# Kernel tuning notes

Hardware: AMD Instinct MI355X
Metric: run time of the kernel (lower is better)

## Reference

```python
import jax, jax.numpy as jnp
import numpy as np

IN_C = 256
INTER_C = 128


def _conv1x1(x_flat, w, b):
    # x_flat: [n, c_in, N]; w: [c_out, c_in]; b: [c_out] -> [n, c_out, N]
    return jnp.einsum('oc,bcn->bon', w, x_flat) + b[None, :, None]


def setup_inputs() -> dict:
    key = jax.random.key(0)
    ks = jax.random.split(key, 9)
    x = jax.random.normal(ks[0], (4, IN_C, 64, 64), dtype=jnp.float32)
    s_in = 1.0 / np.sqrt(IN_C)
    s_mid = 1.0 / np.sqrt(INTER_C)
    return {
        'x': x,
        'g_w': jax.random.uniform(ks[1], (INTER_C, IN_C), jnp.float32, -s_in, s_in),
        'g_b': jax.random.uniform(ks[2], (INTER_C,), jnp.float32, -s_in, s_in),
        'theta_w': jax.random.uniform(ks[3], (INTER_C, IN_C), jnp.float32, -s_in, s_in),
        'theta_b': jax.random.uniform(ks[4], (INTER_C,), jnp.float32, -s_in, s_in),
        'phi_w': jax.random.uniform(ks[5], (INTER_C, IN_C), jnp.float32, -s_in, s_in),
        'phi_b': jax.random.uniform(ks[6], (INTER_C,), jnp.float32, -s_in, s_in),
        'out_w': jax.random.uniform(ks[7], (IN_C, INTER_C), jnp.float32, -s_mid, s_mid),
        'out_b': jax.random.uniform(ks[8], (IN_C,), jnp.float32, -s_mid, s_mid),
    }


def reference(x, g_w, g_b, theta_w, theta_b, phi_w, phi_b, out_w, out_b):
    n, c, h, w = x.shape
    N = h * w
    x_flat = x.reshape(n, c, N)
    # 1x1-conv projections
    g_x = _conv1x1(x_flat, g_w, g_b).transpose(0, 2, 1)       # [n, N, ci]
    theta_x = _conv1x1(x_flat, theta_w, theta_b).transpose(0, 2, 1)  # [n, N, ci]
    phi_x = _conv1x1(x_flat, phi_w, phi_b)                    # [n, ci, N]
    # dot_product variant: pairwise weight normalized by N (no softmax)
    pairwise_weight = jnp.matmul(theta_x, phi_x) / N          # [n, N, N]
    y = jnp.matmul(pairwise_weight, g_x)                      # [n, N, ci]
    y = y.transpose(0, 2, 1)                                  # [n, ci, N]
    out = x_flat + _conv1x1(y, out_w, out_b)                  # residual
    return out.reshape(n, c, h, w)
```

## Files before the change

kernel.cpp:

```cpp
#include <hip/hip_runtime.h>
#include <hip/hip_bf16.h>


#define CC   256
#define NSP  4096
#define NB   4
#define KSPLIT 16

typedef __attribute__((ext_vector_type(8))) short bf16x8;
typedef __attribute__((ext_vector_type(4))) float f32x4;

#define F_WEND 1048576
#define H_PG   0
#define H_TT   4194304
#define H_S2   6291456

__device__ __forceinline__ unsigned short f2bf(float f) {
  __hip_bfloat16 h = __float2bfloat16(f);
  return __builtin_bit_cast(unsigned short, h);
}
__device__ __forceinline__ uint4 pack8(const unsigned short* h) {
  uint4 u;
  u.x = (unsigned)h[0] | ((unsigned)h[1] << 16);
  u.y = (unsigned)h[2] | ((unsigned)h[3] << 16);
  u.z = (unsigned)h[4] | ((unsigned)h[5] << 16);
  u.w = (unsigned)h[6] | ((unsigned)h[7] << 16);
  return u;
}
__device__ __forceinline__ bf16x8 ld_cvt8(const float* __restrict__ p) {
  float4 lo = *(const float4*)p;
  float4 hi = *(const float4*)(p + 4);
  bf16x8 r;
  r[0] = (short)f2bf(lo.x); r[1] = (short)f2bf(lo.y);
  r[2] = (short)f2bf(lo.z); r[3] = (short)f2bf(lo.w);
  r[4] = (short)f2bf(hi.x); r[5] = (short)f2bf(hi.y);
  r[6] = (short)f2bf(hi.z); r[7] = (short)f2bf(hi.w);
  return r;
}

__device__ __forceinline__ void wave_gemm_bt(const unsigned short* __restrict__ A, int pitchA,
                                             const unsigned short* __restrict__ B, int pitchB,
                                             int K, int lane, f32x4 acc[4][4]) {
  int lm = lane & 15, lq = lane >> 4;
  const unsigned short* ap[4];
  const unsigned short* bp[4];
#pragma unroll
  for (int i = 0; i < 4; ++i) {
    ap[i] = A + (size_t)(i * 16 + lm) * pitchA + lq * 8;
    bp[i] = B + (size_t)(i * 16 + lm) * pitchB + lq * 8;
  }
  bf16x8 a0[4], b0[4];
#pragma unroll
  for (int i = 0; i < 4; ++i) {
    a0[i] = *(const bf16x8*)(ap[i]);
    b0[i] = *(const bf16x8*)(bp[i]);
  }
  for (int k = 32; k < K; k += 32) {
    bf16x8 a1[4], b1[4];
#pragma unroll
    for (int i = 0; i < 4; ++i) {
      a1[i] = *(const bf16x8*)(ap[i] + k);
      b1[i] = *(const bf16x8*)(bp[i] + k);
    }
#pragma unroll
    for (int mi = 0; mi < 4; ++mi)
#pragma unroll
      for (int ni = 0; ni < 4; ++ni)
        acc[mi][ni] = __builtin_amdgcn_mfma_f32_16x16x32_bf16(a0[mi], b0[ni], acc[mi][ni], 0, 0, 0);
#pragma unroll
    for (int i = 0; i < 4; ++i) { a0[i] = a1[i]; b0[i] = b1[i]; }
  }
#pragma unroll
  for (int mi = 0; mi < 4; ++mi)
#pragma unroll
    for (int ni = 0; ni < 4; ++ni)
      acc[mi][ni] = __builtin_amdgcn_mfma_f32_16x16x32_bf16(a0[mi], b0[ni], acc[mi][ni], 0, 0, 0);
}

__global__ __launch_bounds__(256) void kP(
    const float* __restrict__ g_w, const float* __restrict__ theta_w,
    const float* __restrict__ phi_w, const float* __restrict__ g_b,
    const float* __restrict__ theta_b, const float* __restrict__ phi_b,
    const float* __restrict__ x, unsigned short* __restrict__ wsh) {
  __shared__ float T[64][65];
  __shared__ unsigned short XL[128 * 256];
  __shared__ float biasL[384];
  int bid = blockIdx.x;
  int b = bid >> 5, c = bid & 31;
  int t = threadIdx.x;
  if (t < 128) {
    biasL[t]       = g_b[t];
    biasL[128 + t] = theta_b[t];
    biasL[256 + t] = phi_b[t];
  }
  for (int s = 0; s < 8; ++s) {
    int kb = s >> 1, nb = s & 1;
    int r = t >> 2, j = t & 3;
    const float* xr = x + ((size_t)b * CC + kb * 64 + r) * NSP + c * 128 + nb * 64 + j * 16;
    float4 f0 = *(const float4*)(xr);
    float4 f1 = *(const float4*)(xr + 4);
    float4 f2 = *(const float4*)(xr + 8);
    float4 f3 = *(const float4*)(xr + 12);
    *(float4*)&T[r][j * 16 + 0]  = f0;
    *(float4*)&T[r][j * 16 + 4]  = f1;
    *(float4*)&T[r][j * 16 + 8]  = f2;
    *(float4*)&T[r][j * 16 + 12] = f3;
    __syncthreads();
    int nr = t >> 2, j2 = t & 3;
    unsigned short o[16];
#pragma unroll
    for (int i = 0; i < 16; ++i) o[i] = f2bf(T[j2 * 16 + i][nr]);
    int row = nb * 64 + nr;
    int kidx = kb * 64 + j2 * 16;
    int sw = (row & 7) << 3;
    *(uint4*)(XL + ((row * 256 + kidx) ^ sw))     = pack8(o);
    *(uint4*)(XL + ((row * 256 + kidx + 8) ^ sw)) = pack8(o + 8);
    __syncthreads();
  }

  int w = t >> 6, lane = t & 63;
  int wm = w >> 1, wn = w & 1;
  int lm = lane & 15, lq = lane >> 4;
  int bsw = (lm & 7) << 3;
#pragma unroll
  for (int r = 0; r < 3; ++r) {
    const float* wptr = (r == 0) ? g_w : (r == 1) ? theta_w : phi_w;
    const float* ap[4];
    int bidx[4];
#pragma unroll
    for (int i = 0; i < 4; ++i) {
      ap[i] = wptr + (size_t)(wm * 64 + i * 16 + lm) * CC + lq * 8;
      bidx[i] = (wn * 64 + i * 16 + lm) * 256 + lq * 8;
    }
    f32x4 acc[4][4] = {};
    bf16x8 a0[4], b0[4];
#pragma unroll
    for (int i = 0; i < 4; ++i) {
      a0[i] = ld_cvt8(ap[i]);
      b0[i] = *(const bf16x8*)(XL + (bidx[i] ^ bsw));
    }
    for (int k = 32; k < 256; k += 32) {
      bf16x8 a1[4], b1[4];
#pragma unroll
      for (int i = 0; i < 4; ++i) {
        a1[i] = ld_cvt8(ap[i] + k);
        b1[i] = *(const bf16x8*)(XL + ((bidx[i] + k) ^ bsw));
      }
#pragma unroll
      for (int mi = 0; mi < 4; ++mi)
#pragma unroll
        for (int ni = 0; ni < 4; ++ni)
          acc[mi][ni] = __builtin_amdgcn_mfma_f32_16x16x32_bf16(a0[mi], b0[ni], acc[mi][ni], 0, 0, 0);
#pragma unroll
      for (int i = 0; i < 4; ++i) { a0[i] = a1[i]; b0[i] = b1[i]; }
    }
#pragma unroll
    for (int mi = 0; mi < 4; ++mi)
#pragma unroll
      for (int ni = 0; ni < 4; ++ni)
        acc[mi][ni] = __builtin_amdgcn_mfma_f32_16x16x32_bf16(a0[mi], b0[ni], acc[mi][ni], 0, 0, 0);

    if (r == 1) {
      size_t tb = (size_t)b * 524288;
#pragma unroll
      for (int mi = 0; mi < 4; ++mi) {
        int p0 = wm * 64 + mi * 16 + lq * 4;
#pragma unroll
        for (int ni = 0; ni < 4; ++ni) {
          int n = c * 128 + wn * 64 + ni * 16 + lm;
          unsigned short u0 = f2bf(acc[mi][ni][0] + biasL[128 + p0 + 0]);
          unsigned short u1 = f2bf(acc[mi][ni][1] + biasL[128 + p0 + 1]);
          unsigned short u2 = f2bf(acc[mi][ni][2] + biasL[128 + p0 + 2]);
          unsigned short u3 = f2bf(acc[mi][ni][3] + biasL[128 + p0 + 3]);
          uint2 o;
          o.x = (unsigned)u0 | ((unsigned)u1 << 16);
          o.y = (unsigned)u2 | ((unsigned)u3 << 16);
          *(uint2*)(wsh + H_TT + tb + (size_t)n * 128 + p0) = o;
        }
      }
    } else {
      int rbase = (r == 0) ? 0 : 128;
      size_t pbo = (size_t)b * 1048576;
#pragma unroll
      for (int mi = 0; mi < 4; ++mi)
#pragma unroll
        for (int rr = 0; rr < 4; ++rr) {
          int rl = wm * 64 + mi * 16 + lq * 4 + rr;
          float bv = biasL[r * 128 + rl];
          size_t rowo = pbo + (size_t)(rbase + rl) * NSP;
#pragma unroll
          for (int ni = 0; ni < 4; ++ni)
            wsh[H_PG + rowo + c * 128 + wn * 64 + ni * 16 + lm] = f2bf(acc[mi][ni][rr] + bv);
        }
    }
  }
}

__global__ __launch_bounds__(256) void kS(const unsigned short* __restrict__ wsh,
                                          float* __restrict__ wsf) {
  int bid = blockIdx.x;
  int b = bid >> 4, ks = bid & 15;
  int t = threadIdx.x, w = t >> 6, lane = t & 63;
  int lm = lane & 15, lq = lane >> 4;
  int qm = w >> 1, qn = w & 1;
  const unsigned short* A = wsh + H_PG + (size_t)b * 1048576 +
                            (size_t)(128 + qm * 64) * NSP + ks * 256;
  const unsigned short* B = wsh + H_PG + (size_t)b * 1048576 +
                            (size_t)(qn * 64) * NSP + ks * 256;
  f32x4 acc[4][4] = {};
  wave_gemm_bt(A, NSP, B, NSP, 256, lane, acc);
  float* P = wsf + (size_t)(b * KSPLIT + ks) * 16384;
#pragma unroll
  for (int mi = 0; mi < 4; ++mi)
#pragma unroll
    for (int rr = 0; rr < 4; ++rr) {
      int p = qm * 64 + mi * 16 + lq * 4 + rr;
#pragma unroll
      for (int ni = 0; ni < 4; ++ni)
        P[p * 128 + qn * 64 + ni * 16 + lm] = acc[mi][ni][rr];
    }
}

__global__ __launch_bounds__(256) void kR(const float* __restrict__ wsf,
                                          unsigned short* __restrict__ wsh) {
  int bid = blockIdx.x;
  int b = bid >> 4, e = bid & 15;
  int t = threadIdx.x;
  int base = e * 1024 + t * 4;
  const float* PB = wsf + (size_t)b * KSPLIT * 16384;
  float4 s = {0.f, 0.f, 0.f, 0.f};
#pragma unroll
  for (int ks = 0; ks < KSPLIT; ++ks) {
    float4 p = *(const float4*)(PB + (size_t)ks * 16384 + base);
    s.x += p.x; s.y += p.y; s.z += p.z; s.w += p.w;
  }
  uint2 o;
  o.x = (unsigned)f2bf(s.x) | ((unsigned)f2bf(s.y) << 16);
  o.y = (unsigned)f2bf(s.z) | ((unsigned)f2bf(s.w) << 16);
  *(uint2*)(wsh + H_S2 + (size_t)b * 16384 + base) = o;
}

__global__ __launch_bounds__(256) void kD(const unsigned short* __restrict__ wsh,
                                          const float* __restrict__ out_w,
                                          const float* __restrict__ x,
                                          const float* __restrict__ out_b,
                                          float* __restrict__ out) {
  __shared__ unsigned short W2L[128 * 128];
  int bid = blockIdx.x;
  int b = bid >> 6, r6 = bid & 63;
  int tm = r6 >> 5, tn = r6 & 31;
  int t = threadIdx.x, w = t >> 6, lane = t & 63;
  int lm = lane & 15, lq = lane >> 4;
  int rb = tm * 128;

  {
    int pm = w >> 1, im = w & 1;
    const unsigned short* As = wsh + H_S2 + (size_t)b * 16384;
    f32x4 macc[4][4] = {};
    for (int kk = 0; kk < 128; kk += 32) {
      bf16x8 a[4], bb[4];
#pragma unroll
      for (int i = 0; i < 4; ++i) {
        a[i]  = *(const bf16x8*)(As + (size_t)(pm * 64 + i * 16 + lm) * 128 + lq * 8 + kk);
        bb[i] = ld_cvt8(out_w + (size_t)(rb + im * 64 + i * 16 + lm) * 128 + lq * 8 + kk);
      }
#pragma unroll
      for (int mi = 0; mi < 4; ++mi)
#pragma unroll
        for (int ni = 0; ni < 4; ++ni)
          macc[mi][ni] = __builtin_amdgcn_mfma_f32_16x16x32_bf16(a[mi], bb[ni], macc[mi][ni], 0, 0, 0);
    }
    const float inv = 1.0f / 4096.0f;
#pragma unroll
    for (int mi = 0; mi < 4; ++mi) {
      int p0 = pm * 64 + mi * 16 + lq * 4;
#pragma unroll
      for (int ni = 0; ni < 4; ++ni) {
        int il = im * 64 + ni * 16 + lm;
        unsigned short u0 = f2bf(macc[mi][ni][0] * inv);
        unsigned short u1 = f2bf(macc[mi][ni][1] * inv);
        unsigned short u2 = f2bf(macc[mi][ni][2] * inv);
        unsigned short u3 = f2bf(macc[mi][ni][3] * inv);
        uint2 o;
        o.x = (unsigned)u0 | ((unsigned)u1 << 16);
        o.y = (unsigned)u2 | ((unsigned)u3 << 16);
        *(uint2*)(W2L + ((il * 128 + p0) ^ ((il & 7) << 3))) = o;
      }
    }
  }
  __syncthreads();

  int wm = w >> 1, wn = w & 1;
  int cb = tn * 128 + wn * 64;
  int asw = (lm & 7) << 3;
  int aidx[4];
  const unsigned short* bp[4];
#pragma unroll
  for (int i = 0; i < 4; ++i) {
    aidx[i] = (wm * 64 + i * 16 + lm) * 128 + lq * 8;
    bp[i] = wsh + H_TT + (size_t)b * 524288 + (size_t)(cb + i * 16 + lm) * 128 + lq * 8;
  }
  f32x4 acc[4][4] = {};
  bf16x8 a0[4], b0[4];
#pragma unroll
  for (int i = 0; i < 4; ++i) {
    a0[i] = *(const bf16x8*)(W2L + (aidx[i] ^ asw));
    b0[i] = *(const bf16x8*)(bp[i]);
  }
  for (int k = 32; k < 128; k += 32) {
    bf16x8 a1[4], b1[4];
#pragma unroll
    for (int i = 0; i < 4; ++i) {
      a1[i] = *(const bf16x8*)(W2L + ((aidx[i] + k) ^ asw));
      b1[i] = *(const bf16x8*)(bp[i] + k);
    }
#pragma unroll
    for (int mi = 0; mi < 4; ++mi)
#pragma unroll
      for (int ni = 0; ni < 4; ++ni)
        acc[mi][ni] = __builtin_amdgcn_mfma_f32_16x16x32_bf16(a0[mi], b0[ni], acc[mi][ni], 0, 0, 0);
#pragma unroll
    for (int i = 0; i < 4; ++i) { a0[i] = a1[i]; b0[i] = b1[i]; }
  }
#pragma unroll
  for (int mi = 0; mi < 4; ++mi)
#pragma unroll
    for (int ni = 0; ni < 4; ++ni)
      acc[mi][ni] = __builtin_amdgcn_mfma_f32_16x16x32_bf16(a0[mi], b0[ni], acc[mi][ni], 0, 0, 0);

#pragma unroll
  for (int mi = 0; mi < 4; ++mi)
#pragma unroll
    for (int rr = 0; rr < 4; ++rr) {
      int row = rb + wm * 64 + mi * 16 + lq * 4 + rr;
      float bi = out_b[row];
#pragma unroll
      for (int ni = 0; ni < 4; ++ni) {
        int col = cb + ni * 16 + lm;
        size_t off = ((size_t)b * CC + row) * NSP + col;
        out[off] = acc[mi][ni][rr] + x[off] + bi;
      }
    }
}

extern "C" void kernel_launch(void* const* d_in, const int* in_sizes, int n_in,
                              void* d_out, int out_size, void* d_ws, size_t ws_size,
                              hipStream_t stream) {
  const float* x       = (const float*)d_in[0];
  const float* g_w     = (const float*)d_in[1];
  const float* g_b     = (const float*)d_in[2];
  const float* theta_w = (const float*)d_in[3];
  const float* theta_b = (const float*)d_in[4];
  const float* phi_w   = (const float*)d_in[5];
  const float* phi_b   = (const float*)d_in[6];
  const float* out_w   = (const float*)d_in[7];
  const float* out_b   = (const float*)d_in[8];
  float* wsf = (float*)d_ws;
  unsigned short* wsh = (unsigned short*)(wsf + F_WEND);
  float* out = (float*)d_out;

  kP<<<dim3(128), dim3(256), 0, stream>>>(g_w, theta_w, phi_w,
                                          g_b, theta_b, phi_b, x, wsh);
  kS<<<dim3(64), dim3(256), 0, stream>>>(wsh, wsf);
  kR<<<dim3(64), dim3(256), 0, stream>>>(wsf, wsh);
  kD<<<dim3(256), dim3(256), 0, stream>>>(wsh, out_w, x, out_b, out);
}
```

Baseline: 138.6 us.

## Fuse phi·g^T partial products into projection kernel, drop separate split-K kernel

The projection kernel now keeps its g and phi tiles in registers, stages them into shared memory, and computes the per-block 128x128 partial of phi·g^T directly, writing fp32 partials (32 splits, one per spatial chunk). This removes the bf16 g/phi round-trip through global memory and one kernel launch. The cost is more fp32 partial data for the reduction kernel to sum (KSPLIT doubles) and extra register and shared-memory pressure in kP.

```diff
diff --git a/kernel.cpp b/kernel.cpp
--- a/kernel.cpp
+++ b/kernel.cpp
@@ -5,15 +5,14 @@
 #define CC   256
 #define NSP  4096
 #define NB   4
-#define KSPLIT 16
+#define KSPLIT 32
 
 typedef __attribute__((ext_vector_type(8))) short bf16x8;
 typedef __attribute__((ext_vector_type(4))) float f32x4;
 
-#define F_WEND 1048576
-#define H_PG   0
-#define H_TT   4194304
-#define H_S2   6291456
+#define F_WEND 2097152
+#define H_TT   0
+#define H_S2   2097152
 
 __device__ __forceinline__ unsigned short f2bf(float f) {
   __hip_bfloat16 h = __float2bfloat16(f);
@@ -38,50 +37,12 @@
   return r;
 }
 
-__device__ __forceinline__ void wave_gemm_bt(const unsigned short* __restrict__ A, int pitchA,
-                                             const unsigned short* __restrict__ B, int pitchB,
-                                             int K, int lane, f32x4 acc[4][4]) {
-  int lm = lane & 15, lq = lane >> 4;
-  const unsigned short* ap[4];
-  const unsigned short* bp[4];
-#pragma unroll
-  for (int i = 0; i < 4; ++i) {
-    ap[i] = A + (size_t)(i * 16 + lm) * pitchA + lq * 8;
-    bp[i] = B + (size_t)(i * 16 + lm) * pitchB + lq * 8;
-  }
-  bf16x8 a0[4], b0[4];
-#pragma unroll
-  for (int i = 0; i < 4; ++i) {
-    a0[i] = *(const bf16x8*)(ap[i]);
-    b0[i] = *(const bf16x8*)(bp[i]);
-  }
-  for (int k = 32; k < K; k += 32) {
-    bf16x8 a1[4], b1[4];
-#pragma unroll
-    for (int i = 0; i < 4; ++i) {
-      a1[i] = *(const bf16x8*)(ap[i] + k);
-      b1[i] = *(const bf16x8*)(bp[i] + k);
-    }
-#pragma unroll
-    for (int mi = 0; mi < 4; ++mi)
-#pragma unroll
-      for (int ni = 0; ni < 4; ++ni)
-        acc[mi][ni] = __builtin_amdgcn_mfma_f32_16x16x32_bf16(a0[mi], b0[ni], acc[mi][ni], 0, 0, 0);
-#pragma unroll
-    for (int i = 0; i < 4; ++i) { a0[i] = a1[i]; b0[i] = b1[i]; }
-  }
-#pragma unroll
-  for (int mi = 0; mi < 4; ++mi)
-#pragma unroll
-    for (int ni = 0; ni < 4; ++ni)
-      acc[mi][ni] = __builtin_amdgcn_mfma_f32_16x16x32_bf16(a0[mi], b0[ni], acc[mi][ni], 0, 0, 0);
-}
-
 __global__ __launch_bounds__(256) void kP(
     const float* __restrict__ g_w, const float* __restrict__ theta_w,
     const float* __restrict__ phi_w, const float* __restrict__ g_b,
     const float* __restrict__ theta_b, const float* __restrict__ phi_b,
-    const float* __restrict__ x, unsigned short* __restrict__ wsh) {
+    const float* __restrict__ x, float* __restrict__ wsf,
+    unsigned short* __restrict__ wsh) {
   __shared__ float T[64][65];
   __shared__ unsigned short XL[128 * 256];
   __shared__ float biasL[384];
@@ -122,6 +83,8 @@
   int wm = w >> 1, wn = w & 1;
   int lm = lane & 15, lq = lane >> 4;
   int bsw = (lm & 7) << 3;
+  uint ygp[4][4][2];
+  uint ypp[4][4][2];
 #pragma unroll
   for (int r = 0; r < 3; ++r) {
     const float* wptr = (r == 0) ? g_w : (r == 1) ? theta_w : phi_w;
@@ -178,47 +141,81 @@
           *(uint2*)(wsh + H_TT + tb + (size_t)n * 128 + p0) = o;
         }
       }
+    } else if (r == 0) {
+#pragma unroll
+      for (int mi = 0; mi < 4; ++mi) {
+        int p0 = wm * 64 + mi * 16 + lq * 4;
+#pragma unroll
+        for (int ni = 0; ni < 4; ++ni) {
+          unsigned short u0 = f2bf(acc[mi][ni][0] + biasL[p0 + 0]);
+          unsigned short u1 = f2bf(acc[mi][ni][1] + biasL[p0 + 1]);
+          unsigned short u2 = f2bf(acc[mi][ni][2] + biasL[p0 + 2]);
+          unsigned short u3 = f2bf(acc[mi][ni][3] + biasL[p0 + 3]);
+          ygp[mi][ni][0] = (unsigned)u0 | ((unsigned)u1 << 16);
+          ygp[mi][ni][1] = (unsigned)u2 | ((unsigned)u3 << 16);
+        }
+      }
     } else {
-      int rbase = (r == 0) ? 0 : 128;
-      size_t pbo = (size_t)b * 1048576;
+#pragma unroll
+      for (int mi = 0; mi < 4; ++mi) {
+        int p0 = wm * 64 + mi * 16 + lq * 4;
+#pragma unroll
+        for (int ni = 0; ni < 4; ++ni) {
+          unsigned short u0 = f2bf(acc[mi][ni][0] + biasL[256 + p0 + 0]);
+          unsigned short u1 = f2bf(acc[mi][ni][1] + biasL[256 + p0 + 1]);
+          unsigned short u2 = f2bf(acc[mi][ni][2] + biasL[256 + p0 + 2]);
+          unsigned short u3 = f2bf(acc[mi][ni][3] + biasL[256 + p0 + 3]);
+          ypp[mi][ni][0] = (unsigned)u0 | ((unsigned)u1 << 16);
+          ypp[mi][ni][1] = (unsigned)u2 | ((unsigned)u3 << 16);
+        }
+      }
+    }
+  }
+
+  __syncthreads();
+#pragma unroll
+  for (int mi = 0; mi < 4; ++mi)
+#pragma unroll
+    for (int ni = 0; ni < 4; ++ni) {
+      int n = wn * 64 + ni * 16 + lm;
+#pragma unroll
+      for (int rr = 0; rr < 4; ++rr) {
+        int p = wm * 64 + mi * 16 + lq * 4 + rr;
+        int phys = (p * 128 + n) ^ ((p & 7) << 3);
+        XL[phys]         = (unsigned short)((ygp[mi][ni][rr >> 1] >> ((rr & 1) * 16)) & 0xFFFF);
+        XL[16384 + phys] = (unsigned short)((ypp[mi][ni][rr >> 1] >> ((rr & 1) * 16)) & 0xFFFF);
+      }
+    }
+  __syncthreads();
+
+  {
+    f32x4 sacc[4][4] = {};
+    for (int k = 0; k < 128; k += 32) {
+      bf16x8 af[4], bg[4];
+#pragma unroll
+      for (int i = 0; i < 4; ++i) {
+        int ra = wm * 64 + i * 16 + lm;
+        int rb2 = wn * 64 + i * 16 + lm;
+        af[i] = *(const bf16x8*)(XL + 16384 + ((ra * 128 + lq * 8 + k) ^ ((ra & 7) << 3)));
+        bg[i] = *(const bf16x8*)(XL + ((rb2 * 128 + lq * 8 + k) ^ ((rb2 & 7) << 3)));
+      }
 #pragma unroll
       for (int mi = 0; mi < 4; ++mi)
 #pragma unroll
-        for (int rr = 0; rr < 4; ++rr) {
-          int rl = wm * 64 + mi * 16 + lq * 4 + rr;
-          float bv = biasL[r * 128 + rl];
-          size_t rowo = pbo + (size_t)(rbase + rl) * NSP;
-#pragma unroll
-          for (int ni = 0; ni < 4; ++ni)
-            wsh[H_PG + rowo + c * 128 + wn * 64 + ni * 16 + lm] = f2bf(acc[mi][ni][rr] + bv);
-        }
-    }
-  }
-}
-
-__global__ __launch_bounds__(256) void kS(const unsigned short* __restrict__ wsh,
-                                          float* __restrict__ wsf) {
-  int bid = blockIdx.x;
-  int b = bid >> 4, ks = bid & 15;
-  int t = threadIdx.x, w = t >> 6, lane = t & 63;
-  int lm = lane & 15, lq = lane >> 4;
-  int qm = w >> 1, qn = w & 1;
-  const unsigned short* A = wsh + H_PG + (size_t)b * 1048576 +
-                            (size_t)(128 + qm * 64) * NSP + ks * 256;
-  const unsigned short* B = wsh + H_PG + (size_t)b * 1048576 +
-                            (size_t)(qn * 64) * NSP + ks * 256;
-  f32x4 acc[4][4] = {};
-  wave_gemm_bt(A, NSP, B, NSP, 256, lane, acc);
-  float* P = wsf + (size_t)(b * KSPLIT + ks) * 16384;
-#pragma unroll
-  for (int mi = 0; mi < 4; ++mi)
-#pragma unroll
-    for (int rr = 0; rr < 4; ++rr) {
-      int p = qm * 64 + mi * 16 + lq * 4 + rr;
-#pragma unroll
-      for (int ni = 0; ni < 4; ++ni)
-        P[p * 128 + qn * 64 + ni * 16 + lm] = acc[mi][ni][rr];
-    }
+        for (int ni = 0; ni < 4; ++ni)
+          sacc[mi][ni] = __builtin_amdgcn_mfma_f32_16x16x32_bf16(af[mi], bg[ni], sacc[mi][ni], 0, 0, 0);
+    }
+    float* P = wsf + (size_t)(b * KSPLIT + c) * 16384;
+#pragma unroll
+    for (int mi = 0; mi < 4; ++mi)
+#pragma unroll
+      for (int rr = 0; rr < 4; ++rr) {
+        int p = wm * 64 + mi * 16 + lq * 4 + rr;
+#pragma unroll
+        for (int ni = 0; ni < 4; ++ni)
+          P[p * 128 + wn * 64 + ni * 16 + lm] = sacc[mi][ni][rr];
+      }
+  }
 }
 
 __global__ __launch_bounds__(256) void kR(const float* __restrict__ wsf,
@@ -360,8 +357,7 @@
   float* out = (float*)d_out;
 
   kP<<<dim3(128), dim3(256), 0, stream>>>(g_w, theta_w, phi_w,
-                                          g_b, theta_b, phi_b, x, wsh);
-  kS<<<dim3(64), dim3(256), 0, stream>>>(wsh, wsf);
+                                          g_b, theta_b, phi_b, x, wsf, wsh);
   kR<<<dim3(64), dim3(256), 0, stream>>>(wsf, wsh);
   kD<<<dim3(256), dim3(256), 0, stream>>>(wsh, out_w, x, out_b, out);
 }
```

Result: faster. 134.8 us (-2.7%).

## Pre-convert projection weights to bf16 and split projection kernel over more blocks

Applied to the files above, without the earlier changes.

Adds a small kernel that converts the g/theta/phi weights to bf16 once per call, so the projection kernel no longer re-reads and converts fp32 weights in every block. The projection kernel now handles 64 spatial columns per block instead of 128, doubling the grid to 256 blocks. Its three projections are fused into one K loop that shares the X tile fragment across all three weight matrices. This costs an extra kernel launch and rearranges the workspace layout, and each block now reads the full bf16 weight set from global memory.

```diff
diff --git a/kernel.cpp b/kernel.cpp
--- a/kernel.cpp
+++ b/kernel.cpp
@@ -11,9 +11,10 @@
 typedef __attribute__((ext_vector_type(4))) float f32x4;
 
 #define F_WEND 1048576
-#define H_PG   0
-#define H_TT   4194304
+#define H_TT   0
+#define H_PG   2097152
 #define H_S2   6291456
+#define H_WH   6356992
 
 __device__ __forceinline__ unsigned short f2bf(float f) {
   __hip_bfloat16 h = __float2bfloat16(f);
@@ -77,26 +78,40 @@
       acc[mi][ni] = __builtin_amdgcn_mfma_f32_16x16x32_bf16(a0[mi], b0[ni], acc[mi][ni], 0, 0, 0);
 }
 
+__global__ __launch_bounds__(256) void kW(const float* __restrict__ g_w,
+                                          const float* __restrict__ theta_w,
+                                          const float* __restrict__ phi_w,
+                                          unsigned short* __restrict__ wsh) {
+  int idx = (blockIdx.x * 256 + threadIdx.x) * 4;
+  int r = idx >> 8;
+  const float* src = (r < 128) ? (g_w + idx)
+                   : (r < 256) ? (theta_w + idx - 32768)
+                               : (phi_w + idx - 65536);
+  float4 v = *(const float4*)src;
+  uint2 o;
+  o.x = (unsigned)f2bf(v.x) | ((unsigned)f2bf(v.y) << 16);
+  o.y = (unsigned)f2bf(v.z) | ((unsigned)f2bf(v.w) << 16);
+  *(uint2*)(wsh + H_WH + idx) = o;
+}
+
 __global__ __launch_bounds__(256) void kP(
-    const float* __restrict__ g_w, const float* __restrict__ theta_w,
-    const float* __restrict__ phi_w, const float* __restrict__ g_b,
-    const float* __restrict__ theta_b, const float* __restrict__ phi_b,
-    const float* __restrict__ x, unsigned short* __restrict__ wsh) {
+    const float* __restrict__ g_b, const float* __restrict__ theta_b,
+    const float* __restrict__ phi_b, const float* __restrict__ x,
+    unsigned short* __restrict__ wsh) {
   __shared__ float T[64][65];
-  __shared__ unsigned short XL[128 * 256];
+  __shared__ unsigned short XL[64 * 256];
   __shared__ float biasL[384];
   int bid = blockIdx.x;
-  int b = bid >> 5, c = bid & 31;
+  int b = bid >> 6, c = bid & 63;
   int t = threadIdx.x;
   if (t < 128) {
     biasL[t]       = g_b[t];
     biasL[128 + t] = theta_b[t];
     biasL[256 + t] = phi_b[t];
   }
-  for (int s = 0; s < 8; ++s) {
-    int kb = s >> 1, nb = s & 1;
+  for (int s = 0; s < 4; ++s) {
     int r = t >> 2, j = t & 3;
-    const float* xr = x + ((size_t)b * CC + kb * 64 + r) * NSP + c * 128 + nb * 64 + j * 16;
+    const float* xr = x + ((size_t)b * CC + s * 64 + r) * NSP + c * 64 + j * 16;
     float4 f0 = *(const float4*)(xr);
     float4 f1 = *(const float4*)(xr + 4);
     float4 f2 = *(const float4*)(xr + 8);
@@ -110,11 +125,10 @@
     unsigned short o[16];
 #pragma unroll
     for (int i = 0; i < 16; ++i) o[i] = f2bf(T[j2 * 16 + i][nr]);
-    int row = nb * 64 + nr;
-    int kidx = kb * 64 + j2 * 16;
-    int sw = (row & 7) << 3;
-    *(uint4*)(XL + ((row * 256 + kidx) ^ sw))     = pack8(o);
-    *(uint4*)(XL + ((row * 256 + kidx + 8) ^ sw)) = pack8(o + 8);
+    int kidx = s * 64 + j2 * 16;
+    int sw = (nr & 7) << 3;
+    *(uint4*)(XL + ((nr * 256 + kidx) ^ sw))     = pack8(o);
+    *(uint4*)(XL + ((nr * 256 + kidx + 8) ^ sw)) = pack8(o + 8);
     __syncthreads();
   }
 
@@ -122,76 +136,59 @@
   int wm = w >> 1, wn = w & 1;
   int lm = lane & 15, lq = lane >> 4;
   int bsw = (lm & 7) << 3;
-#pragma unroll
-  for (int r = 0; r < 3; ++r) {
-    const float* wptr = (r == 0) ? g_w : (r == 1) ? theta_w : phi_w;
-    const float* ap[4];
-    int bidx[4];
+  const unsigned short* aw[4];
+  int bidx[2];
+#pragma unroll
+  for (int i = 0; i < 4; ++i)
+    aw[i] = wsh + H_WH + (size_t)(wm * 64 + i * 16 + lm) * 256 + lq * 8;
+#pragma unroll
+  for (int j = 0; j < 2; ++j)
+    bidx[j] = (wn * 32 + j * 16 + lm) * 256 + lq * 8;
+
+  f32x4 ag[4][2] = {}, at2[4][2] = {}, ap2[4][2] = {};
+#pragma unroll 2
+  for (int k = 0; k < 256; k += 32) {
+    bf16x8 bb[2], xg[4], xt[4], xp[4];
+#pragma unroll
+    for (int j = 0; j < 2; ++j) bb[j] = *(const bf16x8*)(XL + ((bidx[j] + k) ^ bsw));
 #pragma unroll
     for (int i = 0; i < 4; ++i) {
-      ap[i] = wptr + (size_t)(wm * 64 + i * 16 + lm) * CC + lq * 8;
-      bidx[i] = (wn * 64 + i * 16 + lm) * 256 + lq * 8;
-    }
-    f32x4 acc[4][4] = {};
-    bf16x8 a0[4], b0[4];
-#pragma unroll
-    for (int i = 0; i < 4; ++i) {
-      a0[i] = ld_cvt8(ap[i]);
-      b0[i] = *(const bf16x8*)(XL + (bidx[i] ^ bsw));
-    }
-    for (int k = 32; k < 256; k += 32) {
-      bf16x8 a1[4], b1[4];
-#pragma unroll
-      for (int i = 0; i < 4; ++i) {
-        a1[i] = ld_cvt8(ap[i] + k);
-        b1[i] = *(const bf16x8*)(XL + ((bidx[i] + k) ^ bsw));
-      }
-#pragma unroll
-      for (int mi = 0; mi < 4; ++mi)
-#pragma unroll
-        for (int ni = 0; ni < 4; ++ni)
-          acc[mi][ni] = __builtin_amdgcn_mfma_f32_16x16x32_bf16(a0[mi], b0[ni], acc[mi][ni], 0, 0, 0);
-#pragma unroll
-      for (int i = 0; i < 4; ++i) { a0[i] = a1[i]; b0[i] = b1[i]; }
+      xg[i] = *(const bf16x8*)(aw[i] + k);
+      xt[i] = *(const bf16x8*)(aw[i] + 32768 + k);
+      xp[i] = *(const bf16x8*)(aw[i] + 65536 + k);
     }
 #pragma unroll
     for (int mi = 0; mi < 4; ++mi)
 #pragma unroll
-      for (int ni = 0; ni < 4; ++ni)
-        acc[mi][ni] = __builtin_amdgcn_mfma_f32_16x16x32_bf16(a0[mi], b0[ni], acc[mi][ni], 0, 0, 0);
-
-    if (r == 1) {
-      size_t tb = (size_t)b * 524288;
-#pragma unroll
-      for (int mi = 0; mi < 4; ++mi) {
-        int p0 = wm * 64 + mi * 16 + lq * 4;
-#pragma unroll
-        for (int ni = 0; ni < 4; ++ni) {
-          int n = c * 128 + wn * 64 + ni * 16 + lm;
-          unsigned short u0 = f2bf(acc[mi][ni][0] + biasL[128 + p0 + 0]);
-          unsigned short u1 = f2bf(acc[mi][ni][1] + biasL[128 + p0 + 1]);
-          unsigned short u2 = f2bf(acc[mi][ni][2] + biasL[128 + p0 + 2]);
-          unsigned short u3 = f2bf(acc[mi][ni][3] + biasL[128 + p0 + 3]);
-          uint2 o;
-          o.x = (unsigned)u0 | ((unsigned)u1 << 16);
-          o.y = (unsigned)u2 | ((unsigned)u3 << 16);
-          *(uint2*)(wsh + H_TT + tb + (size_t)n * 128 + p0) = o;
-        }
-      }
-    } else {
-      int rbase = (r == 0) ? 0 : 128;
-      size_t pbo = (size_t)b * 1048576;
-#pragma unroll
-      for (int mi = 0; mi < 4; ++mi)
-#pragma unroll
-        for (int rr = 0; rr < 4; ++rr) {
-          int rl = wm * 64 + mi * 16 + lq * 4 + rr;
-          float bv = biasL[r * 128 + rl];
-          size_t rowo = pbo + (size_t)(rbase + rl) * NSP;
-#pragma unroll
-          for (int ni = 0; ni < 4; ++ni)
-            wsh[H_PG + rowo + c * 128 + wn * 64 + ni * 16 + lm] = f2bf(acc[mi][ni][rr] + bv);
-        }
+      for (int ni = 0; ni < 2; ++ni) {
+        ag[mi][ni]  = __builtin_amdgcn_mfma_f32_16x16x32_bf16(xg[mi], bb[ni], ag[mi][ni], 0, 0, 0);
+        at2[mi][ni] = __builtin_amdgcn_mfma_f32_16x16x32_bf16(xt[mi], bb[ni], at2[mi][ni], 0, 0, 0);
+        ap2[mi][ni] = __builtin_amdgcn_mfma_f32_16x16x32_bf16(xp[mi], bb[ni], ap2[mi][ni], 0, 0, 0);
+      }
+  }
+
+  size_t tb = (size_t)b * 524288;
+  size_t pbo = (size_t)b * 1048576;
+#pragma unroll
+  for (int mi = 0; mi < 4; ++mi) {
+    int p0 = wm * 64 + mi * 16 + lq * 4;
+#pragma unroll
+    for (int ni = 0; ni < 2; ++ni) {
+      int n = c * 64 + wn * 32 + ni * 16 + lm;
+      unsigned short u0 = f2bf(at2[mi][ni][0] + biasL[128 + p0 + 0]);
+      unsigned short u1 = f2bf(at2[mi][ni][1] + biasL[128 + p0 + 1]);
+      unsigned short u2 = f2bf(at2[mi][ni][2] + biasL[128 + p0 + 2]);
+      unsigned short u3 = f2bf(at2[mi][ni][3] + biasL[128 + p0 + 3]);
+      uint2 o;
+      o.x = (unsigned)u0 | ((unsigned)u1 << 16);
+      o.y = (unsigned)u2 | ((unsigned)u3 << 16);
+      *(uint2*)(wsh + H_TT + tb + (size_t)n * 128 + p0) = o;
+#pragma unroll
+      for (int rr = 0; rr < 4; ++rr) {
+        int pl = p0 + rr;
+        wsh[H_PG + pbo + (size_t)pl * NSP + n]         = f2bf(ag[mi][ni][rr] + biasL[pl]);
+        wsh[H_PG + pbo + (size_t)(128 + pl) * NSP + n] = f2bf(ap2[mi][ni][rr] + biasL[256 + pl]);
+      }
     }
   }
 }
@@ -359,8 +356,8 @@
   unsigned short* wsh = (unsigned short*)(wsf + F_WEND);
   float* out = (float*)d_out;
 
-  kP<<<dim3(128), dim3(256), 0, stream>>>(g_w, theta_w, phi_w,
-                                          g_b, theta_b, phi_b, x, wsh);
+  kW<<<dim3(96), dim3(256), 0, stream>>>(g_w, theta_w, phi_w, wsh);
+  kP<<<dim3(256), dim3(256), 0, stream>>>(g_b, theta_b, phi_b, x, wsh);
   kS<<<dim3(64), dim3(256), 0, stream>>>(wsh, wsf);
   kR<<<dim3(64), dim3(256), 0, stream>>>(wsf, wsh);
   kD<<<dim3(256), dim3(256), 0, stream>>>(wsh, out_w, x, out_b, out);
```

New measurement: 126.4 us. 1.1x faster.
